# Optimization experiments

Hardware: AMD Instinct MI355X
Metric: run time of the kernel (lower is better)

## Reference

```python
import jax, jax.numpy as jnp
import numpy as np

B, N, W = 4, 16384, 4          # batch, npoints, point feature width (xyz + intensity)
M, K = 512, 32                  # nsample keypoints, neighbors per keypoint
DIL = 2.0
NK = int(K * DIL)               # dilated candidate pool
KG = 8                          # knn size inside DGCNN edge-convs
C3 = 256


def _fps(xyz, m):
    """Farthest point sampling. xyz: (B,N,3) -> indices (B,m)."""
    Bb, Nn, _ = xyz.shape
    def step(carry, _):
        mind, cur = carry
        p = jnp.take_along_axis(xyz, cur[:, None, None], axis=1)  # (B,1,3)
        d = jnp.sum((xyz - p) ** 2, axis=-1)                       # (B,N)
        mind = jnp.minimum(mind, d)
        nxt = jnp.argmax(mind, axis=-1).astype(jnp.int32)
        return (mind, nxt), cur
    init = (jnp.full((Bb, Nn), 1e10, xyz.dtype), jnp.zeros((Bb,), jnp.int32))
    _, idx = jax.lax.scan(step, init, None, length=m)
    return jnp.transpose(idx)  # (B,m)


def _edge_conv(x, w, g, b, kg):
    """Dynamic-graph edge conv. x: (G,P,C) -> (G,P,D). Feature = cat(x_j-x_i, x_i)."""
    sq = jnp.sum(x * x, axis=-1)
    d2 = sq[:, :, None] + sq[:, None, :] - 2.0 * jnp.einsum('gpc,gqc->gpq', x, x)
    _, idx = jax.lax.top_k(-d2, kg)                                   # (G,P,kg)
    xj = jnp.take_along_axis(x[:, None], idx[..., None], axis=2)      # (G,P,kg,C)
    ef = jnp.concatenate([xj - x[:, :, None, :],
                          jnp.broadcast_to(x[:, :, None, :], xj.shape)], axis=-1)
    h = jnp.einsum('gpkc,cd->gpkd', ef, w)
    h = jax.nn.relu(g * h + b)  # BN (inference, unit running stats) + ReLU
    return jnp.max(h, axis=2)   # max over graph neighbors


def setup_inputs() -> dict:
    key = jax.random.key(0)
    ks = jax.random.split(key, 12)
    s = 0.05
    inp = {
        'x': jax.random.normal(ks[0], (B, N, W), jnp.float32),
        'rand_idx': jax.random.randint(ks[1], (K,), 0, NK),
        # DGCNN edge-conv params
        'w_e1': jax.random.normal(ks[2], (24, 64), jnp.float32) * s,
        'g1': jnp.ones((64,), jnp.float32), 'b1': jnp.zeros((64,), jnp.float32),
        'w_e2': jax.random.normal(ks[3], (128, C3), jnp.float32) * s,
        'g2': jnp.ones((C3,), jnp.float32), 'b2': jnp.zeros((C3,), jnp.float32),
        # saliency MLP (1x1 conv1d stacks)
        'w_m1': jax.random.normal(ks[4], (C3, C3), jnp.float32) * s,
        'bm1': jnp.zeros((C3,), jnp.float32),
        'gm1': jnp.ones((C3,), jnp.float32), 'bbm1': jnp.zeros((C3,), jnp.float32),
        'w_m2': jax.random.normal(ks[5], (C3, C3), jnp.float32) * s,
        'bm2': jnp.zeros((C3,), jnp.float32),
        'gm2': jnp.ones((C3,), jnp.float32), 'bbm2': jnp.zeros((C3,), jnp.float32),
        'w_m3': jax.random.normal(ks[6], (C3, 1), jnp.float32) * s,
        'bm3': jnp.zeros((1,), jnp.float32),
    }
    return inp


def reference(x, rand_idx, w_e1, g1, b1, w_e2, g2, b2,
              w_m1, bm1, gm1, bbm1, w_m2, bm2, gm2, bbm2, w_m3, bm3):
    rand_idx = rand_idx.astype(jnp.int32)
    # ---- FPS keypoint sampling ----
    node_idx = _fps(x[:, :, :3], M)                                   # (B,M)
    node = jnp.take_along_axis(x, node_idx[:, :, None], axis=1)       # (B,M,W)
    # ---- random dilation encoding: nk-NN then random k of them ----
    nxyz, pxyz = node[:, :, :3], x[:, :, :3]
    d2 = (jnp.sum(nxyz * nxyz, -1)[:, :, None] + jnp.sum(pxyz * pxyz, -1)[:, None, :]
          - 2.0 * jnp.einsum('bmc,bnc->bmn', nxyz, pxyz))             # (B,M,N)
    _, nn = jax.lax.top_k(-d2, NK)                                    # (B,M,NK)
    sel = nn[:, :, rand_idx]                                          # (B,M,K)
    neigh = jnp.take_along_axis(x[:, None], sel[..., None], axis=2)   # (B,M,K,W)
    rel = neigh[..., :3] - nxyz[:, :, None, :]
    dist = jnp.linalg.norm(rel, axis=-1, keepdims=True)
    node_rep = jnp.broadcast_to(node[:, :, None, :], neigh.shape)
    cluster = jnp.concatenate([node_rep, neigh, rel, dist], axis=-1)  # (B,M,K,12)
    random_cluster = jnp.transpose(cluster, (0, 3, 1, 2))             # (B,12,M,K)
    random_xyz = neigh[..., :3]                                       # (B,M,K,3)
    # ---- DGCNN embedding per cluster ----
    g = cluster.reshape(B * M, K, 12)
    h = _edge_conv(g, w_e1, g1, b1, KG)                               # (BM,K,64)
    h = _edge_conv(h, w_e2, g2, b2, KG)                               # (BM,K,256)
    emb = jnp.transpose(h.reshape(B, M, K, C3), (0, 3, 1, 2))         # (B,256,M,K)
    # ---- attention-weighted pooling ----
    x1 = jnp.max(emb, axis=1)                                         # (B,M,K)
    aw = jax.nn.softmax(x1, axis=-1)
    keypoints = jnp.einsum('bmk,bmkc->bcm', aw, random_xyz)           # (B,3,M)
    afm = emb * aw[:, None]                                           # (B,256,M,K)
    gcf = jnp.sum(afm, axis=-1)                                       # (B,256,M)
    # ---- saliency uncertainty MLP ----
    h = jax.nn.relu(gm1[None, :, None] * (jnp.einsum('bcm,cd->bdm', gcf, w_m1)
                                          + bm1[None, :, None]) + bbm1[None, :, None])
    h = jax.nn.relu(gm2[None, :, None] * (jnp.einsum('bcm,cd->bdm', h, w_m2)
                                          + bm2[None, :, None]) + bbm2[None, :, None])
    s = jnp.einsum('bcm,cd->bdm', h, w_m3) + bm3[None, :, None]       # (B,1,M)
    sal = jax.nn.softplus(s)[:, 0, :] + 0.001                         # (B,M)
    return keypoints, sal, random_cluster, afm
```

## Files before the change

### kernel.cpp

```cpp
#include <hip/hip_runtime.h>
#include <cstdint>

#define Bn 4
#define Nn 16384
#define Mn 512
#define Kn 32

#define O_SAL 6144
#define O_RC  8192
#define O_AFM 794624

__device__ __forceinline__ unsigned fkey(float f) {
  unsigned b = __float_as_uint(f);
  return (b & 0x80000000u) ? ~b : (b | 0x80000000u);
}

__device__ __forceinline__ unsigned long long dkey(double d) {
  unsigned long long b = (unsigned long long)__double_as_longlong(d);
  return (b & 0x8000000000000000ull) ? ~b : (b | 0x8000000000000000ull);
}

__global__ __launch_bounds__(256) void sq_kernel(const float* __restrict__ x,
                                                 float* __restrict__ sqp) {
#pragma clang fp contract(off)
  int i = blockIdx.x * 256 + threadIdx.x;
  float4 v = ((const float4*)x)[i];
  float qx = v.x * v.x;
  float qy = v.y * v.y;
  float qz = v.z * v.z;
  sqp[i] = (qx + qy) + qz;
}

typedef float f2 __attribute__((ext_vector_type(2)));
__device__ __forceinline__ f2 pk_sub(f2 a, f2 b) {
  f2 d;
  asm("v_pk_add_f32 %0, %1, %2 neg_lo:[0,1] neg_hi:[0,1]"
      : "=v"(d) : "v"(a), "v"(b));
  return d;
}
__device__ __forceinline__ f2 pk_mul(f2 a, f2 b) {
  f2 d;
  asm("v_pk_mul_f32 %0, %1, %2" : "=v"(d) : "v"(a), "v"(b));
  return d;
}
__device__ __forceinline__ f2 pk_add(f2 a, f2 b) {
  f2 d;
  asm("v_pk_add_f32 %0, %1, %2" : "=v"(d) : "v"(a), "v"(b));
  return d;
}

template <int CTRL>
__device__ __forceinline__ float dppmaxf(float v) {
  int m = __builtin_amdgcn_update_dpp(__float_as_int(v), __float_as_int(v),
                                      CTRL, 0xf, 0xf, false);
  return fmaxf(v, __int_as_float(m));
}

__global__ __launch_bounds__(1024)
__attribute__((amdgpu_waves_per_eu(4, 4)))
void fps_kernel(const float* __restrict__ x, float* __restrict__ node) {
#pragma clang fp contract(off)
  const int b = blockIdx.x;
  const int t = threadIdx.x;
  const float4* xb = (const float4*)(x + (size_t)b * Nn * 4);
  f2 p2x[8], p2y[8], p2z[8], mind2[8];
  const int base = t * 16;
#pragma unroll
  for (int i = 0; i < 8; ++i) {
    float4 v0 = xb[base + 2 * i];
    float4 v1 = xb[base + 2 * i + 1];
    p2x[i] = (f2){v0.x, v1.x};
    p2y[i] = (f2){v0.y, v1.y};
    p2z[i] = (f2){v0.z, v1.z};
    mind2[i] = (f2){1e10f, 1e10f};
  }
  __shared__ __align__(16) unsigned long long kbuf[2][16];
  float cx, cy, cz;
  {
    float4 v = xb[0];
    cx = v.x; cy = v.y; cz = v.z;
    if (t == 0) ((float4*)node)[b * Mn] = v;
  }
  for (int s = 1; s < Mn; ++s) {
    f2 c2x = (f2){cx, cx}, c2y = (f2){cy, cy}, c2z = (f2){cz, cz};
#pragma unroll
    for (int i = 0; i < 8; ++i) {
      f2 dx = pk_sub(p2x[i], c2x);
      f2 dy = pk_sub(p2y[i], c2y);
      f2 dz = pk_sub(p2z[i], c2z);
      f2 qx = pk_mul(dx, dx);
      f2 qy = pk_mul(dy, dy);
      f2 qz = pk_mul(dz, dz);
      f2 d = pk_add(pk_add(qx, qy), qz);
      mind2[i].x = fminf(mind2[i].x, d.x);
      mind2[i].y = fminf(mind2[i].y, d.y);
    }
    float a0 = fmaxf(mind2[0].x, mind2[0].y);
    float a1 = fmaxf(mind2[1].x, mind2[1].y);
    float a2 = fmaxf(mind2[2].x, mind2[2].y);
    float a3 = fmaxf(mind2[3].x, mind2[3].y);
    float a4 = fmaxf(mind2[4].x, mind2[4].y);
    float a5 = fmaxf(mind2[5].x, mind2[5].y);
    float a6 = fmaxf(mind2[6].x, mind2[6].y);
    float a7 = fmaxf(mind2[7].x, mind2[7].y);
    float b0 = fmaxf(a0, a1);
    float b1 = fmaxf(a2, a3);
    float b2 = fmaxf(a4, a5);
    float b3 = fmaxf(a6, a7);
    float bv = fmaxf(fmaxf(b0, b1), fmaxf(b2, b3));
    int isel = 0;
#pragma unroll
    for (int i = 15; i >= 0; --i) {
      float v = (i & 1) ? mind2[i >> 1].y : mind2[i >> 1].x;
      if (v == bv) isel = i;
    }
    float r = bv;
    r = dppmaxf<0x111>(r);
    r = dppmaxf<0x112>(r);
    r = dppmaxf<0x114>(r);
    r = dppmaxf<0x118>(r);
    r = dppmaxf<0x142>(r);
    r = dppmaxf<0x143>(r);
    float wmax = __int_as_float(__builtin_amdgcn_readlane(__float_as_int(r), 63));
    unsigned long long ball = __ballot(bv == wmax);
    int wl = __ffsll(ball) - 1;
    int widx = __builtin_amdgcn_readlane(base + isel, wl);
    if ((t & 63) == 0) {
      unsigned long long key =
          ((unsigned long long)(__float_as_uint(wmax) | 0x80000000u) << 32) |
          (unsigned)(~widx);
      kbuf[s & 1][t >> 6] = key;
    }
    __syncthreads();
    {
      const unsigned long long* kb = kbuf[s & 1];
      unsigned long long k[16];
#pragma unroll
      for (int w = 0; w < 16; ++w) k[w] = kb[w];
#pragma unroll
      for (int st = 8; st > 0; st >>= 1)
#pragma unroll
        for (int w = 0; w < 8; ++w)
          if (w < st) k[w] = k[w] > k[w + st] ? k[w] : k[w + st];
      int wi = (int)(~(unsigned)(k[0] & 0xFFFFFFFFu));
      float4 nv = xb[wi];
      cx = nv.x; cy = nv.y; cz = nv.z;
      if (t == 0) ((float4*)node)[b * Mn + s] = nv;
    }
  }
}

__global__ __launch_bounds__(256) void knn_kernel(const float* __restrict__ x,
                                                  const float* __restrict__ node,
                                                  const float* __restrict__ sqp,
                                                  const int* __restrict__ rand_idx,
                                                  int* __restrict__ sel) {
#pragma clang fp contract(off)
  const int bm = blockIdx.x;
  const int b = bm >> 9;
  const int t = threadIdx.x;
  const float4* xb = (const float4*)(x + (size_t)b * Nn * 4);
  const float* sq_b = sqp + b * Nn;
  float4 nd = ((const float4*)node)[bm];
  const float nx = nd.x, ny = nd.y, nz = nd.z;
  const float sqmf = (nx * nx + ny * ny) + nz * nz;
  unsigned key[64];
#pragma unroll
  for (int i = 0; i < 64; ++i) {
    int n = t + (i << 8);
    float4 v = xb[n];
    float dot = nx * v.x;
    dot = __builtin_fmaf(ny, v.y, dot);
    dot = __builtin_fmaf(nz, v.z, dot);
    float d2 = (sqmf + sq_b[n]) - 2.0f * dot;
    key[i] = fkey(d2);
  }
  __shared__ unsigned hist[16];
  __shared__ unsigned sh_prefix;
  __shared__ int sh_r;
  unsigned prefix = 0, pmask = 0;
  int r = 95;
  for (int shift = 28; shift >= 0; shift -= 4) {
    if (t < 16) hist[t] = 0;
    __syncthreads();
#pragma unroll
    for (int i = 0; i < 64; ++i) {
      if ((key[i] & pmask) == prefix) atomicAdd(&hist[(key[i] >> shift) & 15], 1u);
    }
    __syncthreads();
    if (t == 0) {
      int rr = r;
      unsigned bin = 0;
      for (unsigned j = 0; j < 16; ++j) {
        int c = (int)hist[j];
        if (rr < c) { bin = j; break; }
        rr -= c;
      }
      sh_prefix = prefix | (bin << shift);
      sh_r = rr;
    }
    __syncthreads();
    prefix = sh_prefix;
    r = sh_r;
    pmask |= (0xFu << shift);
  }
  const unsigned T = prefix;
  __shared__ int cnt;
  __shared__ unsigned long long karr[128];
  if (t == 0) cnt = 0;
  __syncthreads();
#pragma unroll
  for (int i = 0; i < 64; ++i) {
    if (key[i] <= T) {
      int pos = atomicAdd(&cnt, 1);
      if (pos < 128) {
        unsigned n = (unsigned)(t + (i << 8));
        karr[pos] = ((unsigned long long)key[i] << 32) | n;
      }
    }
  }
  __syncthreads();
  const int nc = cnt < 128 ? cnt : 128;
  if (t < 128 && t >= nc) karr[t] = ~0ull;
  for (int k = 2; k <= 128; k <<= 1) {
    for (int j = k >> 1; j > 0; j >>= 1) {
      __syncthreads();
      if (t < 64) {
        int i = ((t & ~(j - 1)) << 1) | (t & (j - 1));
        int ip = i | j;
        unsigned long long ka = karr[i], kb = karr[ip];
        bool asc = ((i & k) == 0);
        if ((ka > kb) == asc) { karr[i] = kb; karr[ip] = ka; }
      }
    }
  }
  __syncthreads();
  if (t < 32) {
    int ri = rand_idx[t];
    sel[bm * 32 + t] = (int)(unsigned)(karr[ri] & 0xFFFFFFFFu);
  }
}

__device__ __forceinline__ void topk8(const unsigned long long* row, unsigned char* nb) {
  unsigned long long bk[8];
  unsigned char bi[8];
#pragma unroll
  for (int k = 0; k < 8; ++k) { bk[k] = ~0ull; bi[k] = 255; }
  for (int q = 0; q < 32; ++q) {
    unsigned long long kv = row[q];
    if (kv < bk[7]) {
      bk[7] = kv; bi[7] = (unsigned char)q;
#pragma unroll
      for (int k = 6; k >= 0; --k) {
        if (bk[k + 1] < bk[k]) {
          unsigned long long tk = bk[k]; bk[k] = bk[k + 1]; bk[k + 1] = tk;
          unsigned char ti = bi[k]; bi[k] = bi[k + 1]; bi[k + 1] = ti;
        }
      }
    }
  }
#pragma unroll
  for (int k = 0; k < 8; ++k) nb[k] = bi[k];
}

__global__ __launch_bounds__(256) void group_kernel(
    const float* __restrict__ x, const float* __restrict__ node,
    const int* __restrict__ sel, const float* __restrict__ w_e1,
    const float* __restrict__ g1, const float* __restrict__ b1,
    const float* __restrict__ w_e2, const float* __restrict__ g2,
    const float* __restrict__ b2, float* __restrict__ out,
    float* __restrict__ gcf) {
#pragma clang fp contract(off)
  const int bm = blockIdx.x;
  const int b = bm >> 9;
  const int m = bm & 511;
  const int t = threadIdx.x;

  __shared__ float cl[32][13];
  __shared__ float h1t[64][36];
  __shared__ float h1p[32][68];
  __shared__ unsigned char nbr[32][8];
  __shared__ double sqs[32];
  __shared__ float part[4][32];
  __shared__ float aws[32];
  __shared__ union U {
    struct {
      unsigned long long keys[32][32];
      float we_a[12][64];
      float we_d[12][64];
      float a1[32][65];
      float cd1[32][65];
    } s;
    float a2[32 * 256];
  } u;

  const float4* xb = (const float4*)(x + (size_t)b * Nn * 4);
  const float4 ndv = ((const float4*)node)[bm];

  if (t < 32) {
    int n = sel[bm * 32 + t];
    float4 v = xb[n];
    float rx = v.x - ndv.x;
    float ry = v.y - ndv.y;
    float rz = v.z - ndv.z;
    float ds = (rx * rx + ry * ry) + rz * rz;
    ds = __fsqrt_rn(ds);
    cl[t][0] = ndv.x; cl[t][1] = ndv.y; cl[t][2] = ndv.z; cl[t][3] = ndv.w;
    cl[t][4] = v.x;   cl[t][5] = v.y;   cl[t][6] = v.z;   cl[t][7] = v.w;
    cl[t][8] = rx;    cl[t][9] = ry;    cl[t][10] = rz;   cl[t][11] = ds;
  }
  for (int i = t; i < 768; i += 256) {
    int row = i >> 6, d = i & 63;
    float wa = w_e1[row * 64 + d];
    float wb = w_e1[(row + 12) * 64 + d];
    u.s.we_a[row][d] = wa;
    u.s.we_d[row][d] = wb - wa;
  }
  __syncthreads();

  for (int i = t; i < 384; i += 256) {
    int c = i >> 5, p = i & 31;
    out[O_RC + (((size_t)(b * 12 + c) * 512) + m) * 32 + p] = cl[p][c];
  }
  if (t < 32) {
    double q[12];
#pragma unroll
    for (int c = 0; c < 12; ++c) {
      double cv = (double)cl[t][c];
      q[c] = cv * cv;
    }
    double s01 = q[0] + q[1];
    double s23 = q[2] + q[3];
    double s45 = q[4] + q[5];
    double s67 = q[6] + q[7];
    double s = (s01 + s23) + (s45 + s67);
    s = s + q[8];
    s = s + q[9];
    s = s + q[10];
    s = s + q[11];
    sqs[t] = s;
  }
  __syncthreads();

  {
    int p = t >> 3, q0 = (t & 7) << 2;
#pragma unroll
    for (int qq = 0; qq < 4; ++qq) {
      int q = q0 + qq;
      double dot = 0.0;
#pragma unroll
      for (int c = 0; c < 12; ++c)
        dot = dot + (double)cl[p][c] * (double)cl[q][c];
      double d2 = (sqs[p] + sqs[q]) - 2.0 * dot;
      u.s.keys[p][q] = dkey(d2);
    }
  }
  __syncthreads();

  if (t < 32) topk8(&u.s.keys[t][0], &nbr[t][0]);
  {
    int d = t & 63, pg = (t >> 6) << 3;
#pragma unroll
    for (int pp = 0; pp < 8; ++pp) {
      int p = pg + pp;
      float aA = 0.f, aD = 0.f;
#pragma unroll
      for (int c = 0; c < 12; ++c) {
        float xv = cl[p][c];
        aA = fmaf(xv, u.s.we_a[c][d], aA);
        aD = fmaf(xv, u.s.we_d[c][d], aD);
      }
      u.s.a1[p][d] = aA;
      u.s.cd1[p][d] = aD;
    }
  }
  __syncthreads();

  {
    int d = t & 63, pg = (t >> 6) << 3;
    float g1v = g1[d], b1v = b1[d];
#pragma unroll
    for (int pp = 0; pp < 8; ++pp) {
      int p = pg + pp;
      float cd = u.s.cd1[p][d];
      float hm = -1e30f;
#pragma unroll
      for (int k = 0; k < 8; ++k) {
        int j = nbr[p][k];
        float hv = fmaf(g1v, u.s.a1[j][d] + cd, b1v);
        hv = fmaxf(hv, 0.f);
        hm = fmaxf(hm, hv);
      }
      h1t[d][p] = hm;
      h1p[p][d] = hm;
    }
  }
  __syncthreads();

  if (t < 32) {
    double r[8];
#pragma unroll
    for (int j = 0; j < 8; ++j) {
      double hv = (double)h1p[t][j];
      r[j] = hv * hv;
    }
#pragma unroll
    for (int blk = 1; blk < 8; ++blk) {
#pragma unroll
      for (int j = 0; j < 8; ++j) {
        double hv = (double)h1p[t][blk * 8 + j];
        r[j] = r[j] + hv * hv;
      }
    }
    double s01 = r[0] + r[1];
    double s23 = r[2] + r[3];
    double s45 = r[4] + r[5];
    double s67 = r[6] + r[7];
    sqs[t] = (s01 + s23) + (s45 + s67);
  }
  __syncthreads();

  {
    int p = t >> 3, q0 = (t & 7) << 2;
#pragma unroll
    for (int qq = 0; qq < 4; ++qq) {
      int q = q0 + qq;
      double dot = 0.0;
      for (int c = 0; c < 64; ++c)
        dot = dot + (double)h1p[p][c] * (double)h1p[q][c];
      double d2 = (sqs[p] + sqs[q]) - 2.0 * dot;
      u.s.keys[p][q] = dkey(d2);
    }
  }
  __syncthreads();

  if (t < 32) topk8(&u.s.keys[t][0], &nbr[t][0]);
  __syncthreads();

  float accD[32];
  float embv[32];
  {
    float accA[32];
#pragma unroll
    for (int p = 0; p < 32; ++p) { accA[p] = 0.f; accD[p] = 0.f; }
    for (int c = 0; c < 64; ++c) {
      float wt = w_e2[c * 256 + t];
      float wb = w_e2[(c + 64) * 256 + t];
      float wd = wb - wt;
      const float4* row = (const float4*)&h1t[c][0];
#pragma unroll
      for (int p4 = 0; p4 < 8; ++p4) {
        float4 hv = row[p4];
        accA[4 * p4 + 0] = fmaf(hv.x, wt, accA[4 * p4 + 0]);
        accA[4 * p4 + 1] = fmaf(hv.y, wt, accA[4 * p4 + 1]);
        accA[4 * p4 + 2] = fmaf(hv.z, wt, accA[4 * p4 + 2]);
        accA[4 * p4 + 3] = fmaf(hv.w, wt, accA[4 * p4 + 3]);
        accD[4 * p4 + 0] = fmaf(hv.x, wd, accD[4 * p4 + 0]);
        accD[4 * p4 + 1] = fmaf(hv.y, wd, accD[4 * p4 + 1]);
        accD[4 * p4 + 2] = fmaf(hv.z, wd, accD[4 * p4 + 2]);
        accD[4 * p4 + 3] = fmaf(hv.w, wd, accD[4 * p4 + 3]);
      }
    }
#pragma unroll
    for (int p = 0; p < 32; ++p) u.a2[p * 256 + t] = accA[p];
  }
  __syncthreads();
  {
    float g2v = g2[t], b2v = b2[t];
#pragma unroll
    for (int p = 0; p < 32; ++p) {
      float cd = accD[p];
      float e = -1e30f;
#pragma unroll
      for (int k = 0; k < 8; ++k) {
        int j = nbr[p][k];
        float hv = fmaf(g2v, u.a2[j * 256 + t] + cd, b2v);
        hv = fmaxf(hv, 0.f);
        e = fmaxf(e, hv);
      }
      embv[p] = e;
    }
  }

#pragma unroll
  for (int p = 0; p < 32; ++p) {
    float v = embv[p];
#pragma unroll
    for (int off = 32; off > 0; off >>= 1) v = fmaxf(v, __shfl_xor(v, off));
    if ((t & 63) == 0) part[t >> 6][p] = v;
  }
  __syncthreads();

  if (t < 32) {
    float x1 = fmaxf(fmaxf(part[0][t], part[1][t]), fmaxf(part[2][t], part[3][t]));
    float mx = x1;
#pragma unroll
    for (int off = 16; off > 0; off >>= 1) mx = fmaxf(mx, __shfl_xor(mx, off));
    float ex = expf(x1 - mx);
    float sm = ex;
#pragma unroll
    for (int off = 16; off > 0; off >>= 1) sm += __shfl_xor(sm, off);
    float aw = ex / sm;
    aws[t] = aw;
#pragma unroll
    for (int c = 0; c < 3; ++c) {
      float kv = aw * cl[t][4 + c];
#pragma unroll
      for (int off = 16; off > 0; off >>= 1) kv += __shfl_xor(kv, off);
      if (t == 0) out[((size_t)(b * 3 + c)) * 512 + m] = kv;
    }
  }
  __syncthreads();

  {
    float gsum = 0.f;
    size_t abase = (size_t)O_AFM + (((size_t)(b * 256 + t)) * 512 + m) * 32;
    float4* ap = (float4*)(out + abase);
#pragma unroll
    for (int p4 = 0; p4 < 8; ++p4) {
      float4 o;
      o.x = embv[4 * p4 + 0] * aws[4 * p4 + 0];
      o.y = embv[4 * p4 + 1] * aws[4 * p4 + 1];
      o.z = embv[4 * p4 + 2] * aws[4 * p4 + 2];
      o.w = embv[4 * p4 + 3] * aws[4 * p4 + 3];
      gsum += o.x; gsum += o.y; gsum += o.z; gsum += o.w;
      ap[p4] = o;
    }
    gcf[((size_t)(b * 256 + t)) * 512 + m] = gsum;
  }
}

__global__ __launch_bounds__(256) void mlp_kernel(
    const float* __restrict__ gcf, const float* __restrict__ w_m1,
    const float* __restrict__ bm1, const float* __restrict__ gm1,
    const float* __restrict__ bbm1, const float* __restrict__ w_m2,
    const float* __restrict__ bm2, const float* __restrict__ gm2,
    const float* __restrict__ bbm2, const float* __restrict__ w_m3,
    const float* __restrict__ bm3, float* __restrict__ out) {
  const int blk = blockIdx.x;
  const int b = blk >> 4;
  const int m0 = (blk & 15) << 5;
  const int t = threadIdx.x;
  __shared__ float sbuf[256 * 36];

#pragma unroll
  for (int i = 0; i < 32; ++i) {
    int c = (t >> 5) + (i << 3);
    int j = t & 31;
    sbuf[c * 36 + j] = gcf[((size_t)(b * 256 + c)) * 512 + m0 + j];
  }
  __syncthreads();

  float acc[32];
#pragma unroll
  for (int j = 0; j < 32; ++j) acc[j] = 0.f;
  for (int c = 0; c < 256; ++c) {
    float wv = w_m1[c * 256 + t];
    const float4* row = (const float4*)&sbuf[c * 36];
#pragma unroll
    for (int j4 = 0; j4 < 8; ++j4) {
      float4 g4 = row[j4];
      acc[4 * j4 + 0] = fmaf(g4.x, wv, acc[4 * j4 + 0]);
      acc[4 * j4 + 1] = fmaf(g4.y, wv, acc[4 * j4 + 1]);
      acc[4 * j4 + 2] = fmaf(g4.z, wv, acc[4 * j4 + 2]);
      acc[4 * j4 + 3] = fmaf(g4.w, wv, acc[4 * j4 + 3]);
    }
  }
  float y[32];
  {
    float gv = gm1[t], bv = bm1[t], bbv = bbm1[t];
#pragma unroll
    for (int j = 0; j < 32; ++j) y[j] = fmaxf(fmaf(gv, acc[j] + bv, bbv), 0.f);
  }
  __syncthreads();
#pragma unroll
  for (int j = 0; j < 32; ++j) sbuf[t * 36 + j] = y[j];
  __syncthreads();

#pragma unroll
  for (int j = 0; j < 32; ++j) acc[j] = 0.f;
  for (int c = 0; c < 256; ++c) {
    float wv = w_m2[c * 256 + t];
    const float4* row = (const float4*)&sbuf[c * 36];
#pragma unroll
    for (int j4 = 0; j4 < 8; ++j4) {
      float4 g4 = row[j4];
      acc[4 * j4 + 0] = fmaf(g4.x, wv, acc[4 * j4 + 0]);
      acc[4 * j4 + 1] = fmaf(g4.y, wv, acc[4 * j4 + 1]);
      acc[4 * j4 + 2] = fmaf(g4.z, wv, acc[4 * j4 + 2]);
      acc[4 * j4 + 3] = fmaf(g4.w, wv, acc[4 * j4 + 3]);
    }
  }
  {
    float gv = gm2[t], bv = bm2[t], bbv = bbm2[t];
#pragma unroll
    for (int j = 0; j < 32; ++j) y[j] = fmaxf(fmaf(gv, acc[j] + bv, bbv), 0.f);
  }
  __syncthreads();
  {
    float w3v = w_m3[t];
#pragma unroll
    for (int j = 0; j < 32; ++j) sbuf[t * 36 + j] = y[j] * w3v;
  }
  __syncthreads();
  if (t < 32) {
    float s = 0.f;
    for (int d = 0; d < 256; ++d) s += sbuf[d * 36 + t];
    s += bm3[0];
    float sal = log1pf(expf(-fabsf(s))) + fmaxf(s, 0.f) + 0.001f;
    out[O_SAL + (size_t)b * 512 + m0 + t] = sal;
  }
}

extern "C" void kernel_launch(void* const* d_in, const int* in_sizes, int n_in,
                              void* d_out, int out_size, void* d_ws, size_t ws_size,
                              hipStream_t stream) {
  (void)in_sizes; (void)n_in; (void)out_size; (void)ws_size;
  const float* x = (const float*)d_in[0];
  const int* rand_idx = (const int*)d_in[1];
  const float* w_e1 = (const float*)d_in[2];
  const float* g1 = (const float*)d_in[3];
  const float* b1 = (const float*)d_in[4];
  const float* w_e2 = (const float*)d_in[5];
  const float* g2 = (const float*)d_in[6];
  const float* b2 = (const float*)d_in[7];
  const float* w_m1 = (const float*)d_in[8];
  const float* bm1 = (const float*)d_in[9];
  const float* gm1 = (const float*)d_in[10];
  const float* bbm1 = (const float*)d_in[11];
  const float* w_m2 = (const float*)d_in[12];
  const float* bm2 = (const float*)d_in[13];
  const float* gm2 = (const float*)d_in[14];
  const float* bbm2 = (const float*)d_in[15];
  const float* w_m3 = (const float*)d_in[16];
  const float* bm3 = (const float*)d_in[17];
  float* out = (float*)d_out;
  char* ws = (char*)d_ws;

  float* node = (float*)ws;
  float* sqp = (float*)(ws + 32768);
  int* sel = (int*)(ws + 32768 + 262144);
  float* gcf = (float*)(ws + 32768 + 262144 + 262144);

  sq_kernel<<<256, 256, 0, stream>>>(x, sqp);
  fps_kernel<<<Bn, 1024, 0, stream>>>(x, node);
  knn_kernel<<<Bn * Mn, 256, 0, stream>>>(x, node, sqp, rand_idx, sel);
  group_kernel<<<Bn * Mn, 256, 0, stream>>>(x, node, sel, w_e1, g1, b1, w_e2,
                                            g2, b2, out, gcf);
  mlp_kernel<<<64, 256, 0, stream>>>(gcf, w_m1, bm1, gm1, bbm1, w_m2, bm2, gm2,
                                     bbm2, w_m3, bm3, out);
}
```

Measured before the change: 1.762 ms.

## Use 8-bit radix select in knn, shuffle reduction in FPS, pad FPS LDS

In the knn kernel, radix selection now uses four passes over 8-bit digits with 256-bin histograms and a two-level bin scan, in place of eight passes over 4-bit digits. This halves the number of barrier-separated rounds. In the FPS kernel, the serial 16-way tree reduction over shared keys becomes a 16-lane xor-shuffle reduction. A large dummy shared array is also declared, forcing LDS allocation that limits occupancy. The wider histogram raises atomic contention and adds an extra scan step.

```diff
diff --git a/kernel.cpp b/kernel.cpp
--- a/kernel.cpp
+++ b/kernel.cpp
@@ -74,7 +74,9 @@
     p2z[i] = (f2){v0.z, v1.z};
     mind2[i] = (f2){1e10f, 1e10f};
   }
-  __shared__ __align__(16) unsigned long long kbuf[2][16];
+  __shared__ __align__(16) unsigned long long kkey[2][16];
+  __shared__ float4 lds_force[5504];
+  if (node == (float*)16) lds_force[t].x = (float)t;
   float cx, cy, cz;
   {
     float4 v = xb[0];
@@ -129,20 +131,17 @@
       unsigned long long key =
           ((unsigned long long)(__float_as_uint(wmax) | 0x80000000u) << 32) |
           (unsigned)(~widx);
-      kbuf[s & 1][t >> 6] = key;
+      kkey[s & 1][t >> 6] = key;
     }
     __syncthreads();
     {
-      const unsigned long long* kb = kbuf[s & 1];
-      unsigned long long k[16];
-#pragma unroll
-      for (int w = 0; w < 16; ++w) k[w] = kb[w];
-#pragma unroll
-      for (int st = 8; st > 0; st >>= 1)
-#pragma unroll
-        for (int w = 0; w < 8; ++w)
-          if (w < st) k[w] = k[w] > k[w + st] ? k[w] : k[w + st];
-      int wi = (int)(~(unsigned)(k[0] & 0xFFFFFFFFu));
+      unsigned long long kk = kkey[s & 1][t & 15];
+#pragma unroll
+      for (int off = 1; off < 16; off <<= 1) {
+        unsigned long long ok = __shfl_xor(kk, off, 16);
+        kk = ok > kk ? ok : kk;
+      }
+      int wi = (int)(~(unsigned)(kk & 0xFFFFFFFFu));
       float4 nv = xb[wi];
       cx = nv.x; cy = nv.y; cz = nv.z;
       if (t == 0) ((float4*)node)[b * Mn + s] = nv;
@@ -175,25 +174,39 @@
     float d2 = (sqmf + sq_b[n]) - 2.0f * dot;
     key[i] = fkey(d2);
   }
-  __shared__ unsigned hist[16];
+  __shared__ unsigned hist[256];
+  __shared__ unsigned gsum[16];
   __shared__ unsigned sh_prefix;
   __shared__ int sh_r;
   unsigned prefix = 0, pmask = 0;
   int r = 95;
-  for (int shift = 28; shift >= 0; shift -= 4) {
-    if (t < 16) hist[t] = 0;
+  for (int shift = 24; shift >= 0; shift -= 8) {
+    hist[t] = 0;
     __syncthreads();
 #pragma unroll
     for (int i = 0; i < 64; ++i) {
-      if ((key[i] & pmask) == prefix) atomicAdd(&hist[(key[i] >> shift) & 15], 1u);
+      if ((key[i] & pmask) == prefix) atomicAdd(&hist[(key[i] >> shift) & 255], 1u);
+    }
+    __syncthreads();
+    if (t < 16) {
+      unsigned ssum = 0;
+#pragma unroll
+      for (int j = 0; j < 16; ++j) ssum += hist[t * 16 + j];
+      gsum[t] = ssum;
     }
     __syncthreads();
     if (t == 0) {
       int rr = r;
-      unsigned bin = 0;
+      unsigned g = 0;
       for (unsigned j = 0; j < 16; ++j) {
-        int c = (int)hist[j];
-        if (rr < c) { bin = j; break; }
+        int c = (int)gsum[j];
+        if (rr < c) { g = j; break; }
+        rr -= c;
+      }
+      unsigned bin = g * 16;
+      for (unsigned j = 0; j < 16; ++j) {
+        int c = (int)hist[g * 16 + j];
+        if (rr < c) { bin = g * 16 + j; break; }
         rr -= c;
       }
       sh_prefix = prefix | (bin << shift);
@@ -202,7 +215,7 @@
     __syncthreads();
     prefix = sh_prefix;
     r = sh_r;
-    pmask |= (0xFu << shift);
+    pmask |= (0xFFu << shift);
   }
   const unsigned T = prefix;
   __shared__ int cnt;
```

Result: faster. 1.709 ms (-3.0%).
